# Optimization experiments

Hardware: AMD Instinct MI355X
Metric: run time of the kernel (lower is better)

## Reference

```python
import jax, jax.numpy as jnp
import numpy as np

HID = 128
CDIM = 128
NCH = 3
NDIM = 3


def _linear_params(key, fan_in, fan_out):
    kw, kb = jax.random.split(key)
    bound = 1.0 / np.sqrt(fan_in)
    W = jax.random.uniform(kw, (fan_in, fan_out), jnp.float32, -bound, bound)
    b = jax.random.uniform(kb, (fan_out,), jnp.float32, -bound, bound)
    return W, b


def setup_inputs() -> dict:
    key = jax.random.key(0)
    keys = jax.random.split(key, 12)
    p = jax.random.normal(keys[0], (32, 8192, NDIM), jnp.float32)
    W_pos, b_pos = _linear_params(keys[1], NDIM, 2 * HID)
    W0, b0 = _linear_params(keys[2], 2 * HID, HID)
    W1, b1 = _linear_params(keys[3], 2 * HID, HID)
    W2, b2 = _linear_params(keys[4], 2 * HID, HID)
    W3, b3 = _linear_params(keys[5], 2 * HID, HID)
    Wc, bc = _linear_params(keys[6], HID, CDIM)
    Wm0, bm0 = _linear_params(keys[7], CDIM, HID)
    Wm1, bm1 = _linear_params(keys[8], HID, HID)
    Wm2, bm2 = _linear_params(keys[9], HID, HID)
    Wp, bp = _linear_params(keys[10], HID, NCH * 3)
    return dict(p=p, W_pos=W_pos, b_pos=b_pos, W0=W0, b0=b0, W1=W1, b1=b1,
                W2=W2, b2=b2, W3=W3, b3=b3, Wc=Wc, bc=bc,
                Wm0=Wm0, bm0=bm0, Wm1=Wm1, bm1=bm1, Wm2=Wm2, bm2=bm2,
                Wp=Wp, bp=bp)


def _relu(x):
    return jnp.maximum(x, 0)


def _pool_cat(net):
    # max over points (dim=1), broadcast back and concat on features
    pooled = jnp.max(net, axis=1, keepdims=True)
    pooled = jnp.broadcast_to(pooled, net.shape)
    return jnp.concatenate([net, pooled], axis=2)  # [B, T, 2*hid]


def reference(p, W_pos, b_pos, W0, b0, W1, b1, W2, b2, W3, b3,
              Wc, bc, Wm0, bm0, Wm1, bm1, Wm2, bm2, Wp, bp):
    net = p @ W_pos + b_pos                      # [B, T, 2*hid]
    net = _relu(net) @ W0 + b0                   # [B, T, hid]
    net = _relu(_pool_cat(net)) @ W1 + b1        # [B, T, hid]
    net = _relu(_pool_cat(net)) @ W2 + b2        # [B, T, hid]
    net = _relu(_pool_cat(net)) @ W3 + b3        # [B, T, hid]
    net = jnp.max(net, axis=1)                   # [B, hid]
    net = _relu(net) @ Wc + bc                   # [B, c_dim]
    net = _relu(net) @ Wm0 + bm0
    net = _relu(net) @ Wm1 + bm1
    net = _relu(net) @ Wm2 + bm2
    net = _relu(net) @ Wp + bp                   # [B, n_channels*3]
    return net
```

## Files before the change

kernel.cpp:

```cpp
#include <hip/hip_runtime.h>


using bf16x8 = __attribute__((ext_vector_type(8))) __bf16;
using u16x8  = __attribute__((ext_vector_type(8))) unsigned short;
using f32x4  = __attribute__((ext_vector_type(4))) float;

__device__ __forceinline__ unsigned short f2bf(float x) {
  __bf16 b = (__bf16)x;
  return __builtin_bit_cast(unsigned short, b);
}

__device__ __forceinline__ f32x4 mfma16(bf16x8 a, bf16x8 b, f32x4 c) {
  return __builtin_amdgcn_mfma_f32_16x16x32_bf16(a, b, c, 0, 0, 0);
}

union FragU { unsigned short us[8]; u16x8 u; bf16x8 v; };

__global__ __launch_bounds__(256) void k_pack_all(
    const float* __restrict__ W0, const float* __restrict__ W1,
    const float* __restrict__ W2, const float* __restrict__ W3,
    unsigned short* __restrict__ Wt) {
  const int blk = blockIdx.x, t = threadIdx.x;
  const float* src; int slot; unsigned short* dst;
  if (blk < 16)      { src = W0; slot = blk * 256 + t;        dst = Wt; }
  else if (blk < 24) { src = W1; slot = (blk - 16) * 256 + t; dst = Wt + 32768; }
  else if (blk < 32) { src = W2; slot = (blk - 24) * 256 + t; dst = Wt + 49152; }
  else               { src = W3; slot = (blk - 32) * 256 + t; dst = Wt + 65536; }
  const int ks = slot >> 9, rem = slot & 511;
  const int nt = rem >> 6, lane = rem & 63;
  const int n = nt * 16 + (lane & 15);
  const int kb = ks * 32 + ((lane >> 4) << 3);
  FragU fr;
#pragma unroll
  for (int j = 0; j < 8; ++j) fr.us[j] = f2bf(src[(kb + j) * 128 + n]);
  reinterpret_cast<u16x8*>(dst)[slot] = fr.u;
}

__device__ __forceinline__ void epilogue_swapped(
    float (*pmaxs)[128], const f32x4 (&acc)[2][8],
    const float* __restrict__ biasvec, int t, int blk,
    unsigned short* __restrict__ h, float* __restrict__ pm, bool write_h) {
  const int w = t >> 6, lane = t & 63, g = lane >> 4, c = lane & 15;
  unsigned short* hblk = h + (size_t)blk * 32768;
#pragma unroll
  for (int nt = 0; nt < 8; ++nt) {
    const float4 bb = *reinterpret_cast<const float4*>(&biasvec[nt * 16 + g * 4]);
    float vm[4] = {0.f, 0.f, 0.f, 0.f};
#pragma unroll
    for (int mi = 0; mi < 2; ++mi) {
      const float v0 = fmaxf(acc[mi][nt][0] + bb.x, 0.f);
      const float v1 = fmaxf(acc[mi][nt][1] + bb.y, 0.f);
      const float v2 = fmaxf(acc[mi][nt][2] + bb.z, 0.f);
      const float v3 = fmaxf(acc[mi][nt][3] + bb.w, 0.f);
      vm[0] = fmaxf(vm[0], v0); vm[1] = fmaxf(vm[1], v1);
      vm[2] = fmaxf(vm[2], v2); vm[3] = fmaxf(vm[3], v3);
      if (write_h) {
        ushort4 s4;
        s4.x = f2bf(v0); s4.y = f2bf(v1); s4.z = f2bf(v2); s4.w = f2bf(v3);
        const int slot = (w * 2 + mi) * 256 + (nt >> 1) * 64 +
                         ((nt & 1) * 2 + (g >> 1)) * 16 + c;
        *reinterpret_cast<ushort4*>(&hblk[slot * 8 + (g & 1) * 4]) = s4;
      }
    }
#pragma unroll
    for (int r = 0; r < 4; ++r) {
      vm[r] = fmaxf(vm[r], __shfl_xor(vm[r], 1, 64));
      vm[r] = fmaxf(vm[r], __shfl_xor(vm[r], 2, 64));
      vm[r] = fmaxf(vm[r], __shfl_xor(vm[r], 4, 64));
      vm[r] = fmaxf(vm[r], __shfl_xor(vm[r], 8, 64));
    }
    if (c == 0) {
#pragma unroll
      for (int r = 0; r < 4; ++r) pmaxs[w][nt * 16 + g * 4 + r] = vm[r];
    }
  }
  __syncthreads();
  if (t < 128) {
    float m = pmaxs[0][t];
#pragma unroll
    for (int i = 1; i < 8; ++i) m = fmaxf(m, pmaxs[i][t]);
    pm[(size_t)blk * 128 + t] = m;
  }
}

__global__ __launch_bounds__(512) void k_layer0(
    const float* __restrict__ p, const float* __restrict__ Wpos,
    const float* __restrict__ bpos, const float* __restrict__ b0,
    const unsigned short* __restrict__ Wt0, unsigned short* __restrict__ h,
    float* __restrict__ pm) {
  __shared__ float wls[1024];
  __shared__ float pmaxs[8][128];
  const int t = threadIdx.x, blk = blockIdx.x;
  for (int i = t; i < 1024; i += 512) wls[i] = (i < 768) ? Wpos[i] : bpos[i - 768];

  const int w = t >> 6, lane = t & 63, g = lane >> 4, c = lane & 15;
  float px[2], py[2], pz[2];
#pragma unroll
  for (int mi = 0; mi < 2; ++mi) {
    const int row = blk * 256 + (w * 2 + mi) * 16 + c;
    px[mi] = p[row * 3 + 0]; py[mi] = p[row * 3 + 1]; pz[mi] = p[row * 3 + 2];
  }

  f32x4 acc[2][8];
#pragma unroll
  for (int mi = 0; mi < 2; ++mi)
#pragma unroll
    for (int nt = 0; nt < 8; ++nt) acc[mi][nt] = f32x4{0.f, 0.f, 0.f, 0.f};
  __syncthreads();

  const bf16x8* Bf = reinterpret_cast<const bf16x8*>(Wt0);
#pragma unroll
  for (int ks = 0; ks < 8; ++ks) {
    FragU a[2];
    const int kb = ks * 32 + g * 8;
#pragma unroll
    for (int mi = 0; mi < 2; ++mi) {
#pragma unroll
      for (int half = 0; half < 2; ++half) {
        const int kq = kb + half * 4;
        const float4 w0 = *reinterpret_cast<const float4*>(&wls[kq]);
        const float4 w1 = *reinterpret_cast<const float4*>(&wls[256 + kq]);
        const float4 w2 = *reinterpret_cast<const float4*>(&wls[512 + kq]);
        const float4 bb = *reinterpret_cast<const float4*>(&wls[768 + kq]);
        a[mi].us[half * 4 + 0] = f2bf(fmaxf(bb.x + px[mi] * w0.x + py[mi] * w1.x + pz[mi] * w2.x, 0.f));
        a[mi].us[half * 4 + 1] = f2bf(fmaxf(bb.y + px[mi] * w0.y + py[mi] * w1.y + pz[mi] * w2.y, 0.f));
        a[mi].us[half * 4 + 2] = f2bf(fmaxf(bb.z + px[mi] * w0.z + py[mi] * w1.z + pz[mi] * w2.z, 0.f));
        a[mi].us[half * 4 + 3] = f2bf(fmaxf(bb.w + px[mi] * w0.w + py[mi] * w1.w + pz[mi] * w2.w, 0.f));
      }
    }
#pragma unroll
    for (int nt = 0; nt < 8; ++nt) {
      const bf16x8 Wf = Bf[(ks * 8 + nt) * 64 + lane];
      acc[0][nt] = mfma16(Wf, a[0].v, acc[0][nt]);
      acc[1][nt] = mfma16(Wf, a[1].v, acc[1][nt]);
    }
  }
  epilogue_swapped(pmaxs, acc, b0, t, blk, h, pm, true);
}

__global__ __launch_bounds__(512) void k_layer(
    const unsigned short* __restrict__ Wta, const float* __restrict__ cvec,
    unsigned short* __restrict__ h, float* __restrict__ pm, int write_h) {
  __shared__ float pmaxs[8][128];
  const int t = threadIdx.x, blk = blockIdx.x;
  const int w = t >> 6, lane = t & 63;
  const int b = blk >> 5;

  f32x4 acc[2][8];
#pragma unroll
  for (int mi = 0; mi < 2; ++mi)
#pragma unroll
    for (int nt = 0; nt < 8; ++nt) acc[mi][nt] = f32x4{0.f, 0.f, 0.f, 0.f};

  const u16x8* hbase = reinterpret_cast<const u16x8*>(h) + (size_t)blk * 4096;
  const bf16x8* Bf = reinterpret_cast<const bf16x8*>(Wta);
#pragma unroll
  for (int ks = 0; ks < 4; ++ks) {
    FragU a0, a1;
    a0.u = hbase[(w * 2 + 0) * 256 + ks * 64 + lane];
    a1.u = hbase[(w * 2 + 1) * 256 + ks * 64 + lane];
#pragma unroll
    for (int nt = 0; nt < 8; ++nt) {
      const bf16x8 Wf = Bf[(ks * 8 + nt) * 64 + lane];
      acc[0][nt] = mfma16(Wf, a0.v, acc[0][nt]);
      acc[1][nt] = mfma16(Wf, a1.v, acc[1][nt]);
    }
  }
  epilogue_swapped(pmaxs, acc, cvec + b * 128, t, blk, h, pm, write_h != 0);
}

__global__ __launch_bounds__(256) void k_combine(
    const float* __restrict__ pm, const float* __restrict__ Wn,
    const float* __restrict__ bn, float* __restrict__ cout) {
  const int b = blockIdx.x, t = threadIdx.x;
  const int f = t & 127, half = t >> 7;
  __shared__ float part[2][128];
  __shared__ float rm[128];
  float m = 0.f;
  for (int i = half * 16; i < half * 16 + 16; ++i)
    m = fmaxf(m, pm[(size_t)(b * 32 + i) * 128 + f]);
  part[half][f] = m;
  __syncthreads();
  if (t < 128) rm[f] = fmaxf(part[0][f], part[1][f]);
  __syncthreads();
  float s = 0.f;
  for (int q = half * 64; q < half * 64 + 64; ++q)
    s += rm[q] * Wn[(128 + q) * 128 + f];
  part[half][f] = s;
  __syncthreads();
  if (t < 128) cout[b * 128 + f] = part[0][f] + part[1][f] + bn[f];
}

__global__ __launch_bounds__(256) void k_final(
    const float* __restrict__ pm3,
    const float* __restrict__ Wc,  const float* __restrict__ bc,
    const float* __restrict__ Wm0, const float* __restrict__ bm0,
    const float* __restrict__ Wm1, const float* __restrict__ bm1,
    const float* __restrict__ Wm2, const float* __restrict__ bm2,
    const float* __restrict__ Wp,  const float* __restrict__ bp,
    float* __restrict__ out) {
  const int b = blockIdx.x, t = threadIdx.x;
  const int f = t & 127, half = t >> 7;
  __shared__ float part[2][128];
  __shared__ float x[128];
  float m = 0.f;
  for (int i = half * 16; i < half * 16 + 16; ++i)
    m = fmaxf(m, pm3[(size_t)(b * 32 + i) * 128 + f]);
  part[half][f] = m;
  __syncthreads();
  if (t < 128) x[f] = fmaxf(part[0][f], part[1][f]);
  __syncthreads();

  const float* Ws[4] = {Wc, Wm0, Wm1, Wm2};
  const float* bs[4] = {bc, bm0, bm1, bm2};
#pragma unroll
  for (int L = 0; L < 4; ++L) {
    float s = 0.f;
    for (int q = half * 64; q < half * 64 + 64; ++q)
      s += x[q] * Ws[L][q * 128 + f];
    part[half][f] = s;
    __syncthreads();
    if (t < 128) x[f] = fmaxf(part[0][f] + part[1][f] + bs[L][f], 0.f);
    __syncthreads();
  }
  if (t < 9) {
    float s = bp[t];
    for (int q = 0; q < 128; ++q) s += x[q] * Wp[q * 9 + t];
    out[b * 9 + t] = s;
  }
}

extern "C" void kernel_launch(void* const* d_in, const int* in_sizes, int n_in,
                              void* d_out, int out_size, void* d_ws, size_t ws_size,
                              hipStream_t stream) {
  const float *p = nullptr, *Wpos = nullptr, *bpos = nullptr;
  const float *Wp = nullptr, *bp = nullptr;
  const float *W256[4] = {}; int nW256 = 0;
  const float *W128[4] = {}; int nW128 = 0;
  const float *B128[8] = {}; int nB128 = 0;
  for (int i = 0; i < n_in; ++i) {
    const float* q = (const float*)d_in[i];
    switch (in_sizes[i]) {
      case 786432: p = q; break;
      case 768:    Wpos = q; break;
      case 256:    bpos = q; break;
      case 1152:   Wp = q; break;
      case 9:      bp = q; break;
      case 32768:  if (nW256 < 4) W256[nW256++] = q; break;
      case 16384:  if (nW128 < 4) W128[nW128++] = q; break;
      case 128:    if (nB128 < 8) B128[nB128++] = q; break;
      default: break;
    }
  }
  const float *W0 = W256[0], *W1 = W256[1], *W2 = W256[2], *W3 = W256[3];
  const float *Wc = W128[0], *Wm0 = W128[1], *Wm1 = W128[2], *Wm2 = W128[3];
  const float *b0 = B128[0], *b1 = B128[1], *b2 = B128[2], *b3 = B128[3];
  const float *bc = B128[4], *bm0 = B128[5], *bm1 = B128[6], *bm2 = B128[7];
  float* out = (float*)d_out;

  char* ws = (char*)d_ws;
  float* pm = (float*)ws;
  float* cv = (float*)(ws + 524288);
  unsigned short* Wt = (unsigned short*)(ws + 524288 + 16384);
  unsigned short* Wt0 = Wt;
  unsigned short* Wt1 = Wt + 32768;
  unsigned short* Wt2 = Wt + 49152;
  unsigned short* Wt3 = Wt + 65536;
  unsigned short* h = Wt + 81920;

  k_pack_all<<<40, 256, 0, stream>>>(W0, W1, W2, W3, Wt);
  k_layer0<<<1024, 512, 0, stream>>>(p, Wpos, bpos, b0, Wt0, h, pm);
  k_combine<<<32, 256, 0, stream>>>(pm, W1, b1, cv);
  k_layer<<<1024, 512, 0, stream>>>(Wt1, cv, h, pm, 1);
  k_combine<<<32, 256, 0, stream>>>(pm, W2, b2, cv);
  k_layer<<<1024, 512, 0, stream>>>(Wt2, cv, h, pm, 1);
  k_combine<<<32, 256, 0, stream>>>(pm, W3, b3, cv);
  k_layer<<<1024, 512, 0, stream>>>(Wt3, cv, h, pm, 0);
  k_final<<<32, 256, 0, stream>>>(pm, Wc, bc, Wm0, bm0, Wm1, bm1, Wm2, bm2, Wp, bp, out);
}
```

Baseline: 186.4 us.

## Split output columns across wave pairs and hold weight fragments in registers

Each block now covers 128 points instead of 256. The 8 waves form 4 row groups by 2 column groups, so each wave computes 32 rows by 64 columns. Weight fragments are preloaded into registers (B[4][4]) before the MMA loop instead of being loaded from global memory inside it, and the grid doubles to 2048 blocks with twice as many partial-max rows. The goal is to halve per-wave accumulator pressure and take weight-load latency off the MFMA chain, raising occupancy. The cost is more partial maxima for the combine kernels and redundant layer-0 position-MLP work across the column groups.

New measurement: 183.5 us. About the same (-1.6%).

```diff
diff --git a/kernel.cpp b/kernel.cpp
--- a/kernel.cpp
+++ b/kernel.cpp
@@ -36,30 +36,32 @@
   reinterpret_cast<u16x8*>(dst)[slot] = fr.u;
 }
 
-__device__ __forceinline__ void epilogue_swapped(
-    float (*pmaxs)[128], const f32x4 (&acc)[2][8],
+__device__ __forceinline__ void epilogue_half(
+    float (*pmaxs)[128], const f32x4 (&acc)[2][4],
     const float* __restrict__ biasvec, int t, int blk,
     unsigned short* __restrict__ h, float* __restrict__ pm, bool write_h) {
   const int w = t >> 6, lane = t & 63, g = lane >> 4, c = lane & 15;
-  unsigned short* hblk = h + (size_t)blk * 32768;
-#pragma unroll
-  for (int nt = 0; nt < 8; ++nt) {
-    const float4 bb = *reinterpret_cast<const float4*>(&biasvec[nt * 16 + g * 4]);
+  const int rowg = w >> 1, colg = w & 1;
+  unsigned short* hout = h + (size_t)blk * 16384;
+#pragma unroll
+  for (int ntl = 0; ntl < 4; ++ntl) {
+    const int ntg = colg * 4 + ntl;
+    const float4 bb = *reinterpret_cast<const float4*>(&biasvec[ntg * 16 + g * 4]);
     float vm[4] = {0.f, 0.f, 0.f, 0.f};
 #pragma unroll
     for (int mi = 0; mi < 2; ++mi) {
-      const float v0 = fmaxf(acc[mi][nt][0] + bb.x, 0.f);
-      const float v1 = fmaxf(acc[mi][nt][1] + bb.y, 0.f);
-      const float v2 = fmaxf(acc[mi][nt][2] + bb.z, 0.f);
-      const float v3 = fmaxf(acc[mi][nt][3] + bb.w, 0.f);
+      const float v0 = fmaxf(acc[mi][ntl][0] + bb.x, 0.f);
+      const float v1 = fmaxf(acc[mi][ntl][1] + bb.y, 0.f);
+      const float v2 = fmaxf(acc[mi][ntl][2] + bb.z, 0.f);
+      const float v3 = fmaxf(acc[mi][ntl][3] + bb.w, 0.f);
       vm[0] = fmaxf(vm[0], v0); vm[1] = fmaxf(vm[1], v1);
       vm[2] = fmaxf(vm[2], v2); vm[3] = fmaxf(vm[3], v3);
       if (write_h) {
         ushort4 s4;
         s4.x = f2bf(v0); s4.y = f2bf(v1); s4.z = f2bf(v2); s4.w = f2bf(v3);
-        const int slot = (w * 2 + mi) * 256 + (nt >> 1) * 64 +
-                         ((nt & 1) * 2 + (g >> 1)) * 16 + c;
-        *reinterpret_cast<ushort4*>(&hblk[slot * 8 + (g & 1) * 4]) = s4;
+        const int slot = (rowg * 2 + mi) * 256 + (ntg >> 1) * 64 +
+                         ((ntg & 1) * 2 + (g >> 1)) * 16 + c;
+        *reinterpret_cast<ushort4*>(&hout[slot * 8 + (g & 1) * 4]) = s4;
       }
     }
 #pragma unroll
@@ -71,14 +73,13 @@
     }
     if (c == 0) {
 #pragma unroll
-      for (int r = 0; r < 4; ++r) pmaxs[w][nt * 16 + g * 4 + r] = vm[r];
+      for (int r = 0; r < 4; ++r) pmaxs[rowg][ntg * 16 + g * 4 + r] = vm[r];
     }
   }
   __syncthreads();
   if (t < 128) {
-    float m = pmaxs[0][t];
-#pragma unroll
-    for (int i = 1; i < 8; ++i) m = fmaxf(m, pmaxs[i][t]);
+    const float m = fmaxf(fmaxf(pmaxs[0][t], pmaxs[1][t]),
+                          fmaxf(pmaxs[2][t], pmaxs[3][t]));
     pm[(size_t)blk * 128 + t] = m;
   }
 }
@@ -89,84 +90,108 @@
     const unsigned short* __restrict__ Wt0, unsigned short* __restrict__ h,
     float* __restrict__ pm) {
   __shared__ float wls[1024];
-  __shared__ float pmaxs[8][128];
+  __shared__ float pmaxs[4][128];
   const int t = threadIdx.x, blk = blockIdx.x;
   for (int i = t; i < 1024; i += 512) wls[i] = (i < 768) ? Wpos[i] : bpos[i - 768];
 
   const int w = t >> 6, lane = t & 63, g = lane >> 4, c = lane & 15;
+  const int rowg = w >> 1, colg = w & 1;
   float px[2], py[2], pz[2];
 #pragma unroll
   for (int mi = 0; mi < 2; ++mi) {
-    const int row = blk * 256 + (w * 2 + mi) * 16 + c;
+    const int row = blk * 128 + rowg * 32 + mi * 16 + c;
     px[mi] = p[row * 3 + 0]; py[mi] = p[row * 3 + 1]; pz[mi] = p[row * 3 + 2];
   }
 
-  f32x4 acc[2][8];
+  f32x4 acc[2][4];
 #pragma unroll
   for (int mi = 0; mi < 2; ++mi)
 #pragma unroll
-    for (int nt = 0; nt < 8; ++nt) acc[mi][nt] = f32x4{0.f, 0.f, 0.f, 0.f};
-  __syncthreads();
+    for (int ntl = 0; ntl < 4; ++ntl) acc[mi][ntl] = f32x4{0.f, 0.f, 0.f, 0.f};
 
   const bf16x8* Bf = reinterpret_cast<const bf16x8*>(Wt0);
-#pragma unroll
-  for (int ks = 0; ks < 8; ++ks) {
-    FragU a[2];
-    const int kb = ks * 32 + g * 8;
-#pragma unroll
-    for (int mi = 0; mi < 2; ++mi) {
-#pragma unroll
-      for (int half = 0; half < 2; ++half) {
-        const int kq = kb + half * 4;
+  bf16x8 B[4][4];
+#pragma unroll
+  for (int ksl = 0; ksl < 4; ++ksl)
+#pragma unroll
+    for (int ntl = 0; ntl < 4; ++ntl)
+      B[ksl][ntl] = Bf[(ksl * 8 + colg * 4 + ntl) * 64 + lane];
+  __syncthreads();
+
+#pragma unroll
+  for (int pass = 0; pass < 2; ++pass) {
+    if (pass == 1) {
+#pragma unroll
+      for (int ksl = 0; ksl < 4; ++ksl)
+#pragma unroll
+        for (int ntl = 0; ntl < 4; ++ntl)
+          B[ksl][ntl] = Bf[((4 + ksl) * 8 + colg * 4 + ntl) * 64 + lane];
+    }
+#pragma unroll
+    for (int ksl = 0; ksl < 4; ++ksl) {
+      const int ks = pass * 4 + ksl;
+      FragU a[2];
+#pragma unroll
+      for (int h2 = 0; h2 < 2; ++h2) {
+        const int kq = ks * 32 + g * 8 + h2 * 4;
         const float4 w0 = *reinterpret_cast<const float4*>(&wls[kq]);
         const float4 w1 = *reinterpret_cast<const float4*>(&wls[256 + kq]);
         const float4 w2 = *reinterpret_cast<const float4*>(&wls[512 + kq]);
         const float4 bb = *reinterpret_cast<const float4*>(&wls[768 + kq]);
-        a[mi].us[half * 4 + 0] = f2bf(fmaxf(bb.x + px[mi] * w0.x + py[mi] * w1.x + pz[mi] * w2.x, 0.f));
-        a[mi].us[half * 4 + 1] = f2bf(fmaxf(bb.y + px[mi] * w0.y + py[mi] * w1.y + pz[mi] * w2.y, 0.f));
-        a[mi].us[half * 4 + 2] = f2bf(fmaxf(bb.z + px[mi] * w0.z + py[mi] * w1.z + pz[mi] * w2.z, 0.f));
-        a[mi].us[half * 4 + 3] = f2bf(fmaxf(bb.w + px[mi] * w0.w + py[mi] * w1.w + pz[mi] * w2.w, 0.f));
+#pragma unroll
+        for (int mi = 0; mi < 2; ++mi) {
+          a[mi].us[h2 * 4 + 0] = f2bf(fmaxf(bb.x + px[mi] * w0.x + py[mi] * w1.x + pz[mi] * w2.x, 0.f));
+          a[mi].us[h2 * 4 + 1] = f2bf(fmaxf(bb.y + px[mi] * w0.y + py[mi] * w1.y + pz[mi] * w2.y, 0.f));
+          a[mi].us[h2 * 4 + 2] = f2bf(fmaxf(bb.z + px[mi] * w0.z + py[mi] * w1.z + pz[mi] * w2.z, 0.f));
+          a[mi].us[h2 * 4 + 3] = f2bf(fmaxf(bb.w + px[mi] * w0.w + py[mi] * w1.w + pz[mi] * w2.w, 0.f));
+        }
       }
-    }
-#pragma unroll
-    for (int nt = 0; nt < 8; ++nt) {
-      const bf16x8 Wf = Bf[(ks * 8 + nt) * 64 + lane];
-      acc[0][nt] = mfma16(Wf, a[0].v, acc[0][nt]);
-      acc[1][nt] = mfma16(Wf, a[1].v, acc[1][nt]);
-    }
-  }
-  epilogue_swapped(pmaxs, acc, b0, t, blk, h, pm, true);
+#pragma unroll
+      for (int ntl = 0; ntl < 4; ++ntl) {
+        acc[0][ntl] = mfma16(B[ksl][ntl], a[0].v, acc[0][ntl]);
+        acc[1][ntl] = mfma16(B[ksl][ntl], a[1].v, acc[1][ntl]);
+      }
+    }
+  }
+  epilogue_half(pmaxs, acc, b0, t, blk, h, pm, true);
 }
 
 __global__ __launch_bounds__(512) void k_layer(
     const unsigned short* __restrict__ Wta, const float* __restrict__ cvec,
     unsigned short* __restrict__ h, float* __restrict__ pm, int write_h) {
-  __shared__ float pmaxs[8][128];
+  __shared__ float pmaxs[4][128];
   const int t = threadIdx.x, blk = blockIdx.x;
   const int w = t >> 6, lane = t & 63;
-  const int b = blk >> 5;
-
-  f32x4 acc[2][8];
+  const int rowg = w >> 1, colg = w & 1;
+  const int b = blk >> 6;
+
+  bf16x8 B[4][4];
+  const bf16x8* Bf = reinterpret_cast<const bf16x8*>(Wta);
+#pragma unroll
+  for (int ks = 0; ks < 4; ++ks)
+#pragma unroll
+    for (int ntl = 0; ntl < 4; ++ntl)
+      B[ks][ntl] = Bf[(ks * 8 + colg * 4 + ntl) * 64 + lane];
+
+  f32x4 acc[2][4];
 #pragma unroll
   for (int mi = 0; mi < 2; ++mi)
 #pragma unroll
-    for (int nt = 0; nt < 8; ++nt) acc[mi][nt] = f32x4{0.f, 0.f, 0.f, 0.f};
-
-  const u16x8* hbase = reinterpret_cast<const u16x8*>(h) + (size_t)blk * 4096;
-  const bf16x8* Bf = reinterpret_cast<const bf16x8*>(Wta);
+    for (int ntl = 0; ntl < 4; ++ntl) acc[mi][ntl] = f32x4{0.f, 0.f, 0.f, 0.f};
+
+  const u16x8* hblk = reinterpret_cast<const u16x8*>(h) + (size_t)blk * 2048;
 #pragma unroll
   for (int ks = 0; ks < 4; ++ks) {
     FragU a0, a1;
-    a0.u = hbase[(w * 2 + 0) * 256 + ks * 64 + lane];
-    a1.u = hbase[(w * 2 + 1) * 256 + ks * 64 + lane];
-#pragma unroll
-    for (int nt = 0; nt < 8; ++nt) {
-      const bf16x8 Wf = Bf[(ks * 8 + nt) * 64 + lane];
-      acc[0][nt] = mfma16(Wf, a0.v, acc[0][nt]);
-      acc[1][nt] = mfma16(Wf, a1.v, acc[1][nt]);
-    }
-  }
-  epilogue_swapped(pmaxs, acc, cvec + b * 128, t, blk, h, pm, write_h != 0);
+    a0.u = hblk[(rowg * 2 + 0) * 256 + ks * 64 + lane];
+    a1.u = hblk[(rowg * 2 + 1) * 256 + ks * 64 + lane];
+#pragma unroll
+    for (int ntl = 0; ntl < 4; ++ntl) {
+      acc[0][ntl] = mfma16(B[ks][ntl], a0.v, acc[0][ntl]);
+      acc[1][ntl] = mfma16(B[ks][ntl], a1.v, acc[1][ntl]);
+    }
+  }
+  epilogue_half(pmaxs, acc, cvec + b * 128, t, blk, h, pm, write_h != 0);
 }
 
 __global__ __launch_bounds__(256) void k_combine(
@@ -177,8 +202,8 @@
   __shared__ float part[2][128];
   __shared__ float rm[128];
   float m = 0.f;
-  for (int i = half * 16; i < half * 16 + 16; ++i)
-    m = fmaxf(m, pm[(size_t)(b * 32 + i) * 128 + f]);
+  for (int i = half * 32; i < half * 32 + 32; ++i)
+    m = fmaxf(m, pm[(size_t)(b * 64 + i) * 128 + f]);
   part[half][f] = m;
   __syncthreads();
   if (t < 128) rm[f] = fmaxf(part[0][f], part[1][f]);
@@ -204,8 +229,8 @@
   __shared__ float part[2][128];
   __shared__ float x[128];
   float m = 0.f;
-  for (int i = half * 16; i < half * 16 + 16; ++i)
-    m = fmaxf(m, pm3[(size_t)(b * 32 + i) * 128 + f]);
+  for (int i = half * 32; i < half * 32 + 32; ++i)
+    m = fmaxf(m, pm3[(size_t)(b * 64 + i) * 128 + f]);
   part[half][f] = m;
   __syncthreads();
   if (t < 128) x[f] = fmaxf(part[0][f], part[1][f]);
@@ -260,8 +285,8 @@
 
   char* ws = (char*)d_ws;
   float* pm = (float*)ws;
-  float* cv = (float*)(ws + 524288);
-  unsigned short* Wt = (unsigned short*)(ws + 524288 + 16384);
+  float* cv = (float*)(ws + 1048576);
+  unsigned short* Wt = (unsigned short*)(ws + 1048576 + 16384);
   unsigned short* Wt0 = Wt;
   unsigned short* Wt1 = Wt + 32768;
   unsigned short* Wt2 = Wt + 49152;
@@ -269,12 +294,12 @@
   unsigned short* h = Wt + 81920;
 
   k_pack_all<<<40, 256, 0, stream>>>(W0, W1, W2, W3, Wt);
-  k_layer0<<<1024, 512, 0, stream>>>(p, Wpos, bpos, b0, Wt0, h, pm);
+  k_layer0<<<2048, 512, 0, stream>>>(p, Wpos, bpos, b0, Wt0, h, pm);
   k_combine<<<32, 256, 0, stream>>>(pm, W1, b1, cv);
-  k_layer<<<1024, 512, 0, stream>>>(Wt1, cv, h, pm, 1);
+  k_layer<<<2048, 512, 0, stream>>>(Wt1, cv, h, pm, 1);
   k_combine<<<32, 256, 0, stream>>>(pm, W2, b2, cv);
-  k_layer<<<1024, 512, 0, stream>>>(Wt2, cv, h, pm, 1);
+  k_layer<<<2048, 512, 0, stream>>>(Wt2, cv, h, pm, 1);
   k_combine<<<32, 256, 0, stream>>>(pm, W3, b3, cv);
-  k_layer<<<1024, 512, 0, stream>>>(Wt3, cv, h, pm, 0);
+  k_layer<<<2048, 512, 0, stream>>>(Wt3, cv, h, pm, 0);
   k_final<<<32, 256, 0, stream>>>(pm, Wc, bc, Wm0, bm0, Wm1, bm1, Wm2, bm2, Wp, bp, out);
 }
```
